# Optimization experiments

Hardware: AMD Instinct MI355X
Metric: run time of the kernel (lower is better)

Reference implementation:

```python
import jax, jax.numpy as jnp
import numpy as np

B, S, D = 32, 577, 768
H, Dh = 12, 64  # num_attention_heads, attention_head_size = pruned_dim // heads


def setup_inputs() -> dict:
    key = jax.random.key(0)
    ks = jax.random.split(key, 7)
    s = 1.0 / np.sqrt(D)
    return {
        "hidden_states": jax.random.normal(ks[0], (B, S, D), dtype=jnp.float32),
        "Wq": jax.random.normal(ks[1], (D, H * Dh), dtype=jnp.float32) * s,
        "bq": jnp.zeros((H * Dh,), dtype=jnp.float32),
        "Wk": jax.random.normal(ks[2], (D, H * Dh), dtype=jnp.float32) * s,
        "bk": jnp.zeros((H * Dh,), dtype=jnp.float32),
        "Wv": jax.random.normal(ks[3], (D, H * Dh), dtype=jnp.float32) * s,
        "bv": jnp.zeros((H * Dh,), dtype=jnp.float32),
    }


def reference(hidden_states, Wq, bq, Wk, bk, Wv, bv):
    def heads(x):  # [B,S,H*Dh] -> [B,H,S,Dh]
        return x.reshape(B, S, H, Dh).transpose(0, 2, 1, 3)

    q = heads(hidden_states @ Wq + bq)
    k = heads(hidden_states @ Wk + bk)
    v = heads(hidden_states @ Wv + bv)

    scale = 1.0 / np.sqrt(Dh)
    scores = jnp.einsum("bhqd,bhkd->bhqk", q, k) * scale  # [B,H,S,S]
    probs = jax.nn.softmax(scores, axis=-1)  # dropout p=0.0 -> identity
    ctx = jnp.einsum("bhqk,bhkd->bhqd", probs, v)  # [B,H,S,Dh]
    ctx = ctx.transpose(0, 2, 1, 3).reshape(B, S, H * Dh)
    return ctx
```

## Files before the change

kernel.cpp:

```cpp
#include <hip/hip_runtime.h>

#define NB 32
#define SEQ 577
#define SP 640
#define DM 768
#define NH 12
#define DH 64
#define NC 10

typedef __attribute__((ext_vector_type(8))) short bf16x8;
typedef __attribute__((ext_vector_type(4))) short bf16x4;
typedef __attribute__((ext_vector_type(4))) float f32x4;
typedef __attribute__((ext_vector_type(2))) unsigned int u32x2;
typedef __attribute__((ext_vector_type(4))) unsigned int u32x4;
typedef unsigned short u16;

__device__ __forceinline__ u16 f2bf(float f) {
  unsigned int u = __builtin_bit_cast(unsigned int, f);
  u += 0x7fffu + ((u >> 16) & 1u);
  return (u16)(u >> 16);
}

__device__ __forceinline__ unsigned int pack_bf2(float a, float b) {
  unsigned int ua = __builtin_bit_cast(unsigned int, a) + 0x8000u;
  unsigned int ub = __builtin_bit_cast(unsigned int, b) + 0x8000u;
  return __builtin_amdgcn_perm(ub, ua, 0x07060302u);
}

__device__ __forceinline__ void g2l16(const void* g, void* lds) {
  __builtin_amdgcn_global_load_lds(
      (const __attribute__((address_space(1))) void*)g,
      (__attribute__((address_space(3))) void*)lds, 16, 0, 0);
}

__global__ void cvt_x_kernel(const float* __restrict__ X, u16* __restrict__ Xb, int n4) {
  int i = blockIdx.x * 256 + threadIdx.x;
  if (i >= n4) return;
  f32x4 v = *reinterpret_cast<const f32x4*>(X + (size_t)i * 4);
  u32x2 p;
  p[0] = (unsigned)f2bf(v[0]) | ((unsigned)f2bf(v[1]) << 16);
  p[1] = (unsigned)f2bf(v[2]) | ((unsigned)f2bf(v[3]) << 16);
  *reinterpret_cast<u32x2*>(Xb + (size_t)i * 4) = p;
}

__global__ void cvt_w_kernel(const float* __restrict__ Wq, const float* __restrict__ Wk,
                             const float* __restrict__ Wv, u16* __restrict__ Wt) {
  int idx = blockIdx.x * 256 + threadIdx.x;
  int m = blockIdx.y;
  const float* W = (m == 0) ? Wq : (m == 1) ? Wk : Wv;
  int k = idx / DM, n = idx - k * DM;
  Wt[(size_t)m * DM * DM + (size_t)n * DM + k] = f2bf(W[idx]);
}

__global__ __launch_bounds__(512, 2)
void qkv_gemm_kernel(const u16* __restrict__ Xb, const u16* __restrict__ Wt,
                     const float* __restrict__ bq, const float* __restrict__ bk,
                     const float* __restrict__ bv,
                     u16* __restrict__ Qw, u16* __restrict__ Kw, u16* __restrict__ Vw) {
  __shared__ alignas(16) u16 As[4][16 * 512];
  __shared__ alignas(16) u16 Bs[4][16 * 512];

  const int tid = threadIdx.x;
  const int lane = tid & 63;
  const int wid = tid >> 6;
  const int wm = wid >> 2, wn = wid & 3;
  const int l15 = lane & 15, lq = lane >> 4;

  const int flat = (blockIdx.z * 3 + blockIdx.y) * 80 + blockIdx.x;
  const int xcd = flat & 7;
  const int j8 = flat >> 3;
  const int xi = j8 / 9;
  const int yz = j8 - xi * 9;
  const int mt = xi * 8 + xcd;
  const int nt = yz % 3;
  const int qkv = yz / 3;

  const u16* Wm = Wt + (size_t)qkv * DM * DM;
  const float* bias = (qkv == 0) ? bq : (qkv == 1) ? bk : bv;

  const u16* gA[2];
  const u16* gB[2];
#pragma unroll
  for (int s = 0; s < 2; ++s) {
    const int e = wid * 2 + s;
    int r = mt * 256 + e * 16 + l15;
    int br = r / SP;
    int tr = r - br * SP;
    if (tr >= SEQ) tr = SEQ - 1;
    gA[s] = Xb + (size_t)(br * SEQ + tr) * DM + lq * 8;
    gB[s] = Wm + (size_t)(nt * 256 + e * 16 + l15) * DM + lq * 8;
  }

  f32x4 acc[8][4];
#pragma unroll
  for (int i = 0; i < 8; ++i)
#pragma unroll
    for (int j = 0; j < 4; ++j)
#pragma unroll
      for (int r = 0; r < 4; ++r) acc[i][j][r] = 0.0f;

  auto stageA = [&](int buf, int kt) {
    g2l16(gA[0] + kt * 32, &As[buf][(wid * 2 + 0) * 512]);
    g2l16(gA[1] + kt * 32, &As[buf][(wid * 2 + 1) * 512]);
  };
  auto stageB = [&](int buf, int kt) {
    g2l16(gB[0] + kt * 32, &Bs[buf][(wid * 2 + 0) * 512]);
    g2l16(gB[1] + kt * 32, &Bs[buf][(wid * 2 + 1) * 512]);
  };

  stageA(0, 0); stageB(0, 0);
  stageA(1, 1); stageB(1, 1);
  stageA(2, 2); stageB(2, 2);
  asm volatile("s_waitcnt vmcnt(8)" ::: "memory");
  __builtin_amdgcn_s_barrier();

  const int NKT = DM / 32;
  for (int kt = 0; kt < NKT; ++kt) {
    const int buf = kt & 3;
    const int nbuf = (kt + 3) & 3;
    const bool more = (kt + 3 < NKT);
    bf16x8 a03[4], bf4[4], a47[4];

#pragma unroll
    for (int i = 0; i < 4; ++i)
      a03[i] = *reinterpret_cast<const bf16x8*>(&As[buf][((wm * 8 + i) * 64 + lane) * 8]);
#pragma unroll
    for (int j = 0; j < 4; ++j)
      bf4[j] = *reinterpret_cast<const bf16x8*>(&Bs[buf][((wn * 4 + j) * 64 + lane) * 8]);
    if (more) stageA(nbuf, kt + 3);
    __builtin_amdgcn_s_barrier();
    __builtin_amdgcn_s_setprio(1);
#pragma unroll
    for (int i = 0; i < 4; ++i)
#pragma unroll
      for (int j = 0; j < 4; ++j)
        acc[i][j] = __builtin_amdgcn_mfma_f32_16x16x32_bf16(a03[i], bf4[j], acc[i][j], 0, 0, 0);
    __builtin_amdgcn_s_setprio(0);
    __builtin_amdgcn_s_barrier();

#pragma unroll
    for (int i = 0; i < 4; ++i)
      a47[i] = *reinterpret_cast<const bf16x8*>(&As[buf][((wm * 8 + 4 + i) * 64 + lane) * 8]);
    if (more) stageB(nbuf, kt + 3);
    if (kt <= NKT - 4) {
      asm volatile("s_waitcnt vmcnt(8)" ::: "memory");
    } else if (kt == NKT - 3) {
      asm volatile("s_waitcnt vmcnt(4)" ::: "memory");
    } else if (kt == NKT - 2) {
      asm volatile("s_waitcnt vmcnt(0)" ::: "memory");
    }
    __builtin_amdgcn_s_barrier();
    __builtin_amdgcn_s_setprio(1);
#pragma unroll
    for (int i = 0; i < 4; ++i)
#pragma unroll
      for (int j = 0; j < 4; ++j)
        acc[4 + i][j] = __builtin_amdgcn_mfma_f32_16x16x32_bf16(a47[i], bf4[j], acc[4 + i][j], 0, 0, 0);
    __builtin_amdgcn_s_setprio(0);
    __builtin_amdgcn_s_barrier();
  }

  const float sfold = 0.18033688011112042f;
#pragma unroll
  for (int j = 0; j < 4; ++j) {
    const int col = nt * 256 + wn * 64 + j * 16 + l15;
    const int h = col >> 6;
    const int d = col & 63;
    const float bb = bias[col];
#pragma unroll
    for (int i = 0; i < 8; ++i) {
      const int rg = mt * 256 + wm * 128 + i * 16 + lq * 4;
      const int br = rg / SP;
      const int tr = rg - br * SP;
      if (qkv == 2) {
        float v0 = acc[i][j][0] + bb, v1 = acc[i][j][1] + bb;
        float v2 = acc[i][j][2] + bb, v3 = acc[i][j][3] + bb;
        u32x2 p;
        p[0] = (unsigned)f2bf(v0) | ((unsigned)f2bf(v1) << 16);
        p[1] = (unsigned)f2bf(v2) | ((unsigned)f2bf(v3) << 16);
        size_t o = ((size_t)(br * NH + h) * DH + d) * SP + tr;
        *reinterpret_cast<u32x2*>(Vw + o) = p;
      } else {
        u16* dst = ((qkv == 0) ? Qw : Kw) + ((size_t)(br * NH + h) * SP + tr) * DH + d;
#pragma unroll
        for (int r = 0; r < 4; ++r) {
          float v = acc[i][j][r] + bb;
          if (qkv == 0) v *= sfold;
          dst[r * DH] = f2bf(v);
        }
      }
    }
  }
}

#if __has_builtin(__builtin_amdgcn_mfma_f32_16x16x16bf16_1k)
#define MFMA16(a, b, c) __builtin_amdgcn_mfma_f32_16x16x16bf16_1k(a, b, c, 0, 0, 0)
#define HAVE_MFMA16 1
#elif __has_builtin(__builtin_amdgcn_mfma_f32_16x16x16_bf16)
#define MFMA16(a, b, c) __builtin_amdgcn_mfma_f32_16x16x16_bf16(a, b, c, 0, 0, 0)
#define HAVE_MFMA16 1
#else
#define HAVE_MFMA16 0
#endif

__global__ __launch_bounds__(256)
void attn_kernel(const u16* __restrict__ Qw, const u16* __restrict__ Kw,
                 const u16* __restrict__ Vw, float* __restrict__ out) {
  __shared__ alignas(16) u16 Kc[2][8 * 64 * 8];
  __shared__ alignas(16) u16 Vc[2][16 * 64 * 4];

  const int tid = threadIdx.x;
  const int lane = tid & 63;
  const int wid = tid >> 6;
  const int l15 = lane & 15, lq = lane >> 4;

  const int flat = blockIdx.y * 5 + blockIdx.x;
  const int w = (flat & 7) * 240 + (flat >> 3);
  const int qx = w % 5;
  const int bh = w / 5;
  const int b = bh / NH;
  const int h = bh - b * NH;
  const int q0 = qx * 128 + wid * 32;

  const u16* Qb = Qw + (size_t)bh * SP * DH;
  const u16* Kb = Kw + (size_t)bh * SP * DH;
  const u16* Vb = Vw + (size_t)bh * DH * SP;

  bf16x8 qf[2][2];
#pragma unroll
  for (int qt = 0; qt < 2; ++qt)
#pragma unroll
    for (int hf = 0; hf < 2; ++hf)
      qf[qt][hf] = *reinterpret_cast<const bf16x8*>(
          &Qb[(q0 + qt * 16 + l15) * DH + hf * 32 + lq * 8]);

  const u16* gK = Kb + (size_t)(wid * 16 + l15) * DH + lq * 8;
  const u16* gV = Vb + (size_t)(wid * 16 + l15) * SP + lq * 4;

  float mrow[2] = {-__builtin_inff(), -__builtin_inff()};
  float lrow[2] = {0.0f, 0.0f};
  f32x4 acc[2][4];
#pragma unroll
  for (int qt = 0; qt < 2; ++qt)
#pragma unroll
    for (int dt = 0; dt < 4; ++dt)
#pragma unroll
      for (int r = 0; r < 4; ++r) acc[qt][dt][r] = 0.0f;

  g2l16(gK, &Kc[0][(wid * 2 + 0) * 512]);
  g2l16(gK + 32, &Kc[0][(wid * 2 + 1) * 512]);
  {
    u32x2 v[4];
#pragma unroll
    for (int t = 0; t < 4; ++t)
      v[t] = *reinterpret_cast<const u32x2*>(gV + t * 16);
#pragma unroll
    for (int t = 0; t < 4; ++t)
      *reinterpret_cast<u32x2*>(&Vc[0][((wid * 4 + t) * 64 + lane) * 4]) = v[t];
  }
  __syncthreads();

  for (int c = 0; c < NC; ++c) {
    const int cur = c & 1;
    const int c0 = c * 64;
    u32x2 vn[4];
    if (c + 1 < NC) {
      const u16* gKn = gK + (size_t)(c0 + 64) * DH;
      g2l16(gKn, &Kc[cur ^ 1][(wid * 2 + 0) * 512]);
      g2l16(gKn + 32, &Kc[cur ^ 1][(wid * 2 + 1) * 512]);
#pragma unroll
      for (int t = 0; t < 4; ++t)
        vn[t] = *reinterpret_cast<const u32x2*>(gV + (c0 + 64) + t * 16);
    }

    f32x4 s[2][4];
    __builtin_amdgcn_s_setprio(1);
#pragma unroll
    for (int t = 0; t < 4; ++t) {
      bf16x8 kf0 = *reinterpret_cast<const bf16x8*>(&Kc[cur][((t * 2 + 0) * 64 + lane) * 8]);
      bf16x8 kf1 = *reinterpret_cast<const bf16x8*>(&Kc[cur][((t * 2 + 1) * 64 + lane) * 8]);
#pragma unroll
      for (int qt = 0; qt < 2; ++qt) {
        f32x4 z;
#pragma unroll
        for (int r = 0; r < 4; ++r) z[r] = 0.0f;
        z = __builtin_amdgcn_mfma_f32_16x16x32_bf16(kf0, qf[qt][0], z, 0, 0, 0);
        z = __builtin_amdgcn_mfma_f32_16x16x32_bf16(kf1, qf[qt][1], z, 0, 0, 0);
        s[qt][t] = z;
      }
    }
    __builtin_amdgcn_s_setprio(0);
    if (c0 + 64 > SEQ) {
#pragma unroll
      for (int qt = 0; qt < 2; ++qt)
#pragma unroll
        for (int t = 0; t < 4; ++t)
#pragma unroll
          for (int r = 0; r < 4; ++r) {
            int key = c0 + t * 16 + lq * 4 + r;
            s[qt][t][r] = (key < SEQ) ? s[qt][t][r] : -__builtin_inff();
          }
    }
    float alpha[2];
    unsigned int pku[2][4][2];
#pragma unroll
    for (int qt = 0; qt < 2; ++qt) {
      float mx = s[qt][0][0];
#pragma unroll
      for (int t = 0; t < 4; ++t)
#pragma unroll
        for (int r = 0; r < 4; ++r) mx = fmaxf(mx, s[qt][t][r]);
      mx = fmaxf(mx, __shfl_xor(mx, 16));
      mx = fmaxf(mx, __shfl_xor(mx, 32));
      float mn = fmaxf(mrow[qt], mx);
      alpha[qt] = __builtin_amdgcn_exp2f(mrow[qt] - mn);
      mrow[qt] = mn;
      float sm = 0.0f;
#pragma unroll
      for (int t = 0; t < 4; ++t) {
        float p0 = __builtin_amdgcn_exp2f(s[qt][t][0] - mn);
        float p1 = __builtin_amdgcn_exp2f(s[qt][t][1] - mn);
        float p2 = __builtin_amdgcn_exp2f(s[qt][t][2] - mn);
        float p3 = __builtin_amdgcn_exp2f(s[qt][t][3] - mn);
        sm += (p0 + p1) + (p2 + p3);
        pku[qt][t][0] = pack_bf2(p0, p1);
        pku[qt][t][1] = pack_bf2(p2, p3);
      }
      sm += __shfl_xor(sm, 16);
      sm += __shfl_xor(sm, 32);
      lrow[qt] = lrow[qt] * alpha[qt] + sm;
    }

#if HAVE_MFMA16
    __builtin_amdgcn_s_setprio(1);
#pragma unroll
    for (int dt = 0; dt < 4; ++dt) {
      bf16x4 vf[4];
#pragma unroll
      for (int t = 0; t < 4; ++t)
        vf[t] = *reinterpret_cast<const bf16x4*>(&Vc[cur][((dt * 4 + t) * 64 + lane) * 4]);
#pragma unroll
      for (int qt = 0; qt < 2; ++qt) {
        f32x4 a = acc[qt][dt];
#pragma unroll
        for (int r = 0; r < 4; ++r) a[r] *= alpha[qt];
#pragma unroll
        for (int t = 0; t < 4; ++t) {
          bf16x4 pf = __builtin_bit_cast(bf16x4, u32x2{pku[qt][t][0], pku[qt][t][1]});
          a = MFMA16(vf[t], pf, a);
        }
        acc[qt][dt] = a;
      }
    }
    __builtin_amdgcn_s_setprio(0);
#else
#pragma unroll
    for (int qt = 0; qt < 2; ++qt) {
      unsigned int bfrag[2][4];
#pragma unroll
      for (int hh = 0; hh < 2; ++hh)
#pragma unroll
        for (int w2 = 0; w2 < 4; ++w2) {
          int srcl = l15 + 16 * (2 * (lq & 1) + (w2 >> 1));
          unsigned int lo = (unsigned int)__shfl((int)pku[qt][2 * hh][w2 & 1], srcl);
          unsigned int hi = (unsigned int)__shfl((int)pku[qt][2 * hh + 1][w2 & 1], srcl);
          bfrag[hh][w2] = (lq < 2) ? lo : hi;
        }
#pragma unroll
      for (int dt = 0; dt < 4; ++dt) {
        f32x4 a = acc[qt][dt];
#pragma unroll
        for (int r = 0; r < 4; ++r) a[r] *= alpha[qt];
#pragma unroll
        for (int hh = 0; hh < 2; ++hh) {
          u32x2 w0 = *reinterpret_cast<const u32x2*>(&Vc[cur][((dt * 4 + 2 * hh) * 64 + lane) * 4]);
          u32x2 w1 = *reinterpret_cast<const u32x2*>(&Vc[cur][((dt * 4 + 2 * hh + 1) * 64 + lane) * 4]);
          u32x4 vw = {w0[0], w0[1], w1[0], w1[1]};
          u32x4 pw = {bfrag[hh][0], bfrag[hh][1], bfrag[hh][2], bfrag[hh][3]};
          a = __builtin_amdgcn_mfma_f32_16x16x32_bf16(
              __builtin_bit_cast(bf16x8, vw), __builtin_bit_cast(bf16x8, pw), a, 0, 0, 0);
        }
        acc[qt][dt] = a;
      }
    }
#endif

    if (c + 1 < NC) {
#pragma unroll
      for (int t = 0; t < 4; ++t)
        *reinterpret_cast<u32x2*>(&Vc[cur ^ 1][((wid * 4 + t) * 64 + lane) * 4]) = vn[t];
    }
    __syncthreads();
  }

#pragma unroll
  for (int qt = 0; qt < 2; ++qt) {
    int q = q0 + qt * 16 + l15;
    if (q < SEQ) {
      float rl = 1.0f / lrow[qt];
      float* orow = out + ((size_t)b * SEQ + q) * DM + h * DH;
#pragma unroll
      for (int dt = 0; dt < 4; ++dt) {
        f32x4 v = acc[qt][dt];
#pragma unroll
        for (int r = 0; r < 4; ++r) v[r] *= rl;
        *reinterpret_cast<f32x4*>(&orow[dt * 16 + lq * 4]) = v;
      }
    }
  }
}

extern "C" void kernel_launch(void* const* d_in, const int* in_sizes, int n_in,
                              void* d_out, int out_size, void* d_ws, size_t ws_size,
                              hipStream_t stream) {
  (void)in_sizes; (void)n_in; (void)out_size; (void)ws_size;
  const float* X  = (const float*)d_in[0];
  const float* Wq = (const float*)d_in[1];
  const float* bq = (const float*)d_in[2];
  const float* Wk = (const float*)d_in[3];
  const float* bk = (const float*)d_in[4];
  const float* Wv = (const float*)d_in[5];
  const float* bv = (const float*)d_in[6];
  float* out = (float*)d_out;

  char* ws = (char*)d_ws;
  u16* Xb = (u16*)ws;
  u16* Wt = (u16*)(ws + 28366848);
  u16* Qw = (u16*)(ws + 28366848 + 3538944);
  u16* Kw = Qw + (size_t)NB * NH * SP * DH;
  u16* Vw = Kw + (size_t)NB * NH * SP * DH;

  cvt_x_kernel<<<dim3(13848), 256, 0, stream>>>(X, Xb, 3545088);
  cvt_w_kernel<<<dim3(2304, 3), 256, 0, stream>>>(Wq, Wk, Wv, Wt);
  qkv_gemm_kernel<<<dim3(80, 3, 3), 512, 0, stream>>>(Xb, Wt, bq, bk, bv, Qw, Kw, Vw);
  attn_kernel<<<dim3(5, NB * NH), 256, 0, stream>>>(Qw, Kw, Vw, out);
}
```

Baseline: 326.6 us.

## Stage GEMM epilogue through LDS for coalesced stores; tile weight transpose

The QKV GEMM epilogue now writes bias-added bf16 results into a padded shared-memory tile (transposed for V) and then emits 16-byte coalesced global stores, replacing scattered 2-byte and 8-byte stores. The weight conversion kernel becomes a 64x64 tiled transpose through LDS, so both reads and writes are coalesced. To make qkv uniform per launch, the single 720-block GEMM launch is split into three 240-block launches. The larger shared buffer (about 135 KB) may limit occupancy, and the three launches add launch overhead and possible tail effects.

```diff
diff --git a/kernel.cpp b/kernel.cpp
--- a/kernel.cpp
+++ b/kernel.cpp
@@ -43,22 +43,40 @@
   *reinterpret_cast<u32x2*>(Xb + (size_t)i * 4) = p;
 }
 
-__global__ void cvt_w_kernel(const float* __restrict__ Wq, const float* __restrict__ Wk,
-                             const float* __restrict__ Wv, u16* __restrict__ Wt) {
-  int idx = blockIdx.x * 256 + threadIdx.x;
-  int m = blockIdx.y;
+__global__ __launch_bounds__(256)
+void cvt_w_kernel(const float* __restrict__ Wq, const float* __restrict__ Wk,
+                  const float* __restrict__ Wv, u16* __restrict__ Wt) {
+  __shared__ u16 ld[64 * 72];
+  const int m = blockIdx.z;
   const float* W = (m == 0) ? Wq : (m == 1) ? Wk : Wv;
-  int k = idx / DM, n = idx - k * DM;
-  Wt[(size_t)m * DM * DM + (size_t)n * DM + k] = f2bf(W[idx]);
+  const int k0 = blockIdx.y * 64, n0 = blockIdx.x * 64;
+  const int tid = threadIdx.x;
+  const int kr = tid >> 4, c4 = tid & 15;
+#pragma unroll
+  for (int p = 0; p < 4; ++p) {
+    const int k = p * 16 + kr;
+    f32x4 v = *reinterpret_cast<const f32x4*>(&W[(size_t)(k0 + k) * DM + n0 + c4 * 4]);
+#pragma unroll
+    for (int e = 0; e < 4; ++e) ld[(c4 * 4 + e) * 72 + k] = f2bf(v[e]);
+  }
+  __syncthreads();
+  u16* dst = Wt + (size_t)m * DM * DM;
+#pragma unroll
+  for (int p = 0; p < 2; ++p) {
+    const int s = p * 256 + tid;
+    const int n = s >> 3, ch = (s & 7) * 8;
+    u32x4 w = *reinterpret_cast<const u32x4*>(&ld[n * 72 + ch]);
+    *reinterpret_cast<u32x4*>(&dst[(size_t)(n0 + n) * DM + k0 + ch]) = w;
+  }
 }
 
 __global__ __launch_bounds__(512, 2)
 void qkv_gemm_kernel(const u16* __restrict__ Xb, const u16* __restrict__ Wt,
                      const float* __restrict__ bq, const float* __restrict__ bk,
                      const float* __restrict__ bv,
-                     u16* __restrict__ Qw, u16* __restrict__ Kw, u16* __restrict__ Vw) {
-  __shared__ alignas(16) u16 As[4][16 * 512];
-  __shared__ alignas(16) u16 Bs[4][16 * 512];
+                     u16* __restrict__ Qw, u16* __restrict__ Kw, u16* __restrict__ Vw,
+                     const int qkv) {
+  __shared__ alignas(16) u16 sh[256 * 264];
 
   const int tid = threadIdx.x;
   const int lane = tid & 63;
@@ -66,14 +84,12 @@
   const int wm = wid >> 2, wn = wid & 3;
   const int l15 = lane & 15, lq = lane >> 4;
 
-  const int flat = (blockIdx.z * 3 + blockIdx.y) * 80 + blockIdx.x;
+  const int flat = blockIdx.y * 80 + blockIdx.x;
   const int xcd = flat & 7;
   const int j8 = flat >> 3;
-  const int xi = j8 / 9;
-  const int yz = j8 - xi * 9;
+  const int xi = j8 / 3;
+  const int nt = j8 - xi * 3;
   const int mt = xi * 8 + xcd;
-  const int nt = yz % 3;
-  const int qkv = yz / 3;
 
   const u16* Wm = Wt + (size_t)qkv * DM * DM;
   const float* bias = (qkv == 0) ? bq : (qkv == 1) ? bk : bv;
@@ -100,12 +116,12 @@
       for (int r = 0; r < 4; ++r) acc[i][j][r] = 0.0f;
 
   auto stageA = [&](int buf, int kt) {
-    g2l16(gA[0] + kt * 32, &As[buf][(wid * 2 + 0) * 512]);
-    g2l16(gA[1] + kt * 32, &As[buf][(wid * 2 + 1) * 512]);
+    g2l16(gA[0] + kt * 32, &sh[buf * 8192 + (wid * 2 + 0) * 512]);
+    g2l16(gA[1] + kt * 32, &sh[buf * 8192 + (wid * 2 + 1) * 512]);
   };
   auto stageB = [&](int buf, int kt) {
-    g2l16(gB[0] + kt * 32, &Bs[buf][(wid * 2 + 0) * 512]);
-    g2l16(gB[1] + kt * 32, &Bs[buf][(wid * 2 + 1) * 512]);
+    g2l16(gB[0] + kt * 32, &sh[32768 + buf * 8192 + (wid * 2 + 0) * 512]);
+    g2l16(gB[1] + kt * 32, &sh[32768 + buf * 8192 + (wid * 2 + 1) * 512]);
   };
 
   stageA(0, 0); stageB(0, 0);
@@ -123,10 +139,10 @@
 
 #pragma unroll
     for (int i = 0; i < 4; ++i)
-      a03[i] = *reinterpret_cast<const bf16x8*>(&As[buf][((wm * 8 + i) * 64 + lane) * 8]);
+      a03[i] = *reinterpret_cast<const bf16x8*>(&sh[buf * 8192 + ((wm * 8 + i) * 64 + lane) * 8]);
 #pragma unroll
     for (int j = 0; j < 4; ++j)
-      bf4[j] = *reinterpret_cast<const bf16x8*>(&Bs[buf][((wn * 4 + j) * 64 + lane) * 8]);
+      bf4[j] = *reinterpret_cast<const bf16x8*>(&sh[32768 + buf * 8192 + ((wn * 4 + j) * 64 + lane) * 8]);
     if (more) stageA(nbuf, kt + 3);
     __builtin_amdgcn_s_barrier();
     __builtin_amdgcn_s_setprio(1);
@@ -140,7 +156,7 @@
 
 #pragma unroll
     for (int i = 0; i < 4; ++i)
-      a47[i] = *reinterpret_cast<const bf16x8*>(&As[buf][((wm * 8 + 4 + i) * 64 + lane) * 8]);
+      a47[i] = *reinterpret_cast<const bf16x8*>(&sh[buf * 8192 + ((wm * 8 + 4 + i) * 64 + lane) * 8]);
     if (more) stageB(nbuf, kt + 3);
     if (kt <= NKT - 4) {
       asm volatile("s_waitcnt vmcnt(8)" ::: "memory");
@@ -163,32 +179,46 @@
   const float sfold = 0.18033688011112042f;
 #pragma unroll
   for (int j = 0; j < 4; ++j) {
-    const int col = nt * 256 + wn * 64 + j * 16 + l15;
-    const int h = col >> 6;
-    const int d = col & 63;
-    const float bb = bias[col];
+    const int col = wn * 64 + j * 16 + l15;
+    const float bb = bias[nt * 256 + col];
 #pragma unroll
     for (int i = 0; i < 8; ++i) {
-      const int rg = mt * 256 + wm * 128 + i * 16 + lq * 4;
-      const int br = rg / SP;
-      const int tr = rg - br * SP;
+      const int row = wm * 128 + i * 16 + lq * 4;
       if (qkv == 2) {
-        float v0 = acc[i][j][0] + bb, v1 = acc[i][j][1] + bb;
-        float v2 = acc[i][j][2] + bb, v3 = acc[i][j][3] + bb;
-        u32x2 p;
-        p[0] = (unsigned)f2bf(v0) | ((unsigned)f2bf(v1) << 16);
-        p[1] = (unsigned)f2bf(v2) | ((unsigned)f2bf(v3) << 16);
-        size_t o = ((size_t)(br * NH + h) * DH + d) * SP + tr;
-        *reinterpret_cast<u32x2*>(Vw + o) = p;
+        unsigned p0 = (unsigned)f2bf(acc[i][j][0] + bb) | ((unsigned)f2bf(acc[i][j][1] + bb) << 16);
+        unsigned p1 = (unsigned)f2bf(acc[i][j][2] + bb) | ((unsigned)f2bf(acc[i][j][3] + bb) << 16);
+        *reinterpret_cast<u32x2*>(&sh[col * 264 + row]) = u32x2{p0, p1};
       } else {
-        u16* dst = ((qkv == 0) ? Qw : Kw) + ((size_t)(br * NH + h) * SP + tr) * DH + d;
 #pragma unroll
         for (int r = 0; r < 4; ++r) {
           float v = acc[i][j][r] + bb;
           if (qkv == 0) v *= sfold;
-          dst[r * DH] = f2bf(v);
+          sh[(row + r) * 264 + col] = f2bf(v);
         }
       }
+    }
+  }
+  __builtin_amdgcn_s_barrier();
+
+#pragma unroll
+  for (int p = 0; p < 16; ++p) {
+    const int slot = p * 512 + tid;
+    const int rr = slot >> 5;
+    const int cc = (slot & 31) * 8;
+    u32x4 w = *reinterpret_cast<const u32x4*>(&sh[rr * 264 + cc]);
+    if (qkv == 2) {
+      const int gcol = nt * 256 + rr;
+      const int h = gcol >> 6, d = gcol & 63;
+      const int rg = mt * 256 + cc;
+      const int br = rg / SP, tr = rg - br * SP;
+      *reinterpret_cast<u32x4*>(&Vw[((size_t)(br * NH + h) * DH + d) * SP + tr]) = w;
+    } else {
+      const int rg = mt * 256 + rr;
+      const int br = rg / SP, tr = rg - br * SP;
+      const int gcol = nt * 256 + cc;
+      const int h = gcol >> 6, d = gcol & 63;
+      u16* dst = ((qkv == 0) ? Qw : Kw) + ((size_t)(br * NH + h) * SP + tr) * DH + d;
+      *reinterpret_cast<u32x4*>(dst) = w;
     }
   }
 }
@@ -431,7 +461,9 @@
   u16* Vw = Kw + (size_t)NB * NH * SP * DH;
 
   cvt_x_kernel<<<dim3(13848), 256, 0, stream>>>(X, Xb, 3545088);
-  cvt_w_kernel<<<dim3(2304, 3), 256, 0, stream>>>(Wq, Wk, Wv, Wt);
-  qkv_gemm_kernel<<<dim3(80, 3, 3), 512, 0, stream>>>(Xb, Wt, bq, bk, bv, Qw, Kw, Vw);
+  cvt_w_kernel<<<dim3(12, 12, 3), 256, 0, stream>>>(Wq, Wk, Wv, Wt);
+  qkv_gemm_kernel<<<dim3(80, 3), 512, 0, stream>>>(Xb, Wt, bq, bk, bv, Qw, Kw, Vw, 0);
+  qkv_gemm_kernel<<<dim3(80, 3), 512, 0, stream>>>(Xb, Wt, bq, bk, bv, Qw, Kw, Vw, 1);
+  qkv_gemm_kernel<<<dim3(80, 3), 512, 0, stream>>>(Xb, Wt, bq, bk, bv, Qw, Kw, Vw, 2);
   attn_kernel<<<dim3(5, NB * NH), 256, 0, stream>>>(Qw, Kw, Vw, out);
 }
```

Measured after the change: 307.1 us. -6.0%, faster.
